# Kernel optimization log

Hardware: AMD Instinct MI355X
Metric: run time of the kernel (lower is better)

## Reference

```python
import jax, jax.numpy as jnp
import numpy as np

D_STATE = 64
D_CONV = 4
DT_RANK = 16  # ceil(256/16)
LN_EPS = 1e-5


def _mamba_layer(x, ln_g, ln_b, in_w, conv_w, conv_b, xp_w, dt_w, dt_b, A_log, Dp, out_w):
    B, L, d_model = x.shape
    # LayerNorm (pre-norm)
    mu = x.mean(-1, keepdims=True)
    var = ((x - mu) ** 2).mean(-1, keepdims=True)
    xn = (x - mu) * jax.lax.rsqrt(var + LN_EPS) * ln_g + ln_b
    # in_proj -> split into x-branch and gate z
    xz = xn @ in_w.T                    # [B,L,2*d_inner]
    xm, z = jnp.split(xz, 2, axis=-1)   # each [B,L,d_inner]
    d_inner = xm.shape[-1]
    # causal depthwise conv1d (kernel D_CONV), then SiLU
    xp = jnp.pad(xm, ((0, 0), (D_CONV - 1, 0), (0, 0)))
    xc = conv_b + sum(xp[:, k:k + L, :] * conv_w[:, k] for k in range(D_CONV))
    xc = jax.nn.silu(xc)
    # input-dependent SSM params
    dbl = xc @ xp_w.T                   # [B,L,dt_rank+2*N]
    dt, Bm, Cm = jnp.split(dbl, [DT_RANK, DT_RANK + D_STATE], axis=-1)
    dt = jax.nn.softplus(dt @ dt_w.T + dt_b)   # [B,L,d_inner]
    A = -jnp.exp(A_log)                 # [d_inner, N]

    def step(h, inp):
        dt_t, B_t, C_t, u_t = inp       # [B,Di],[B,N],[B,N],[B,Di]
        dA = jnp.exp(dt_t[:, :, None] * A)                 # [B,Di,N]
        dBu = (dt_t * u_t)[:, :, None] * B_t[:, None, :]   # [B,Di,N]
        h = dA * h + dBu
        y = jnp.einsum('bdn,bn->bd', h, C_t)
        return h, y

    h0 = jnp.zeros((B, d_inner, D_STATE), x.dtype)
    _, ys = jax.lax.scan(
        step, h0,
        (dt.transpose(1, 0, 2), Bm.transpose(1, 0, 2), Cm.transpose(1, 0, 2), xc.transpose(1, 0, 2)))
    y = ys.transpose(1, 0, 2) + xc * Dp  # skip term D*u
    y = y * jax.nn.silu(z)               # gating
    out = y @ out_w.T                    # out_proj
    return out + x                       # residual


def reference(x, ln_g, ln_b, in_w, conv_w, conv_b, xp_w, dt_w, dt_b, A_log, Dp, out_w):
    depth = ln_g.shape[0]
    for i in range(depth):
        x = _mamba_layer(x, ln_g[i], ln_b[i], in_w[i], conv_w[i], conv_b[i],
                         xp_w[i], dt_w[i], dt_b[i], A_log[i], Dp[i], out_w[i])
    return x


def setup_inputs() -> dict:
    key = jax.random.key(0)
    ks = jax.random.split(key, 8)
    B, L, d_model, depth = 4, 1024, 256, 2
    d_inner = 2 * d_model
    x = jax.random.normal(ks[0], (B, L, d_model), jnp.float32)
    s = 0.02
    in_w = jax.random.normal(ks[1], (depth, 2 * d_inner, d_model), jnp.float32) * s
    conv_w = jax.random.normal(ks[2], (depth, d_inner, D_CONV), jnp.float32) * 0.3
    conv_b = jnp.zeros((depth, d_inner), jnp.float32)
    xp_w = jax.random.normal(ks[3], (depth, DT_RANK + 2 * D_STATE, d_inner), jnp.float32) * s
    dt_w = jax.random.normal(ks[4], (depth, d_inner, DT_RANK), jnp.float32) * 0.1
    # inverse-softplus of ~0.01 so dt starts small (mamba-style init)
    dt_b = jnp.full((depth, d_inner), float(np.log(np.expm1(0.01))), jnp.float32)
    # A = diag(1..N) per channel -> A_log = log(arange)
    A_log = jnp.broadcast_to(jnp.log(jnp.arange(1, D_STATE + 1, dtype=jnp.float32)),
                             (depth, d_inner, D_STATE))
    Dp = jnp.ones((depth, d_inner), jnp.float32)
    out_w = jax.random.normal(ks[5], (depth, d_model, d_inner), jnp.float32) * s
    ln_g = jnp.ones((depth, d_model), jnp.float32)
    ln_b = jnp.zeros((depth, d_model), jnp.float32)
    return {"x": x, "ln_g": ln_g, "ln_b": ln_b, "in_w": in_w, "conv_w": conv_w,
            "conv_b": conv_b, "xp_w": xp_w, "dt_w": dt_w, "dt_b": dt_b,
            "A_log": A_log, "Dp": Dp, "out_w": out_w}
```

## Files before the change

### kernel.cpp

```cpp
#include <hip/hip_runtime.h>
#include <math.h>

#define DI 512
#define DM 256
#define LSEQ 1024
#define BB 4
#define NST 64
#define ROWS (BB*LSEQ)
#define NC 16
#define CL 64

typedef __bf16 bf16x8 __attribute__((ext_vector_type(8)));
typedef __bf16 bf16x4 __attribute__((ext_vector_type(4)));
typedef float f32x4 __attribute__((ext_vector_type(4)));
typedef unsigned short u16;
typedef u16 u16x8 __attribute__((ext_vector_type(8)));

__device__ __forceinline__ float siluf(float x) { return x / (1.f + __expf(-x)); }
__device__ __forceinline__ float softplusf(float x) { return (x > 20.f) ? x : log1pf(__expf(x)); }
__device__ __forceinline__ float rlane(float v, int l) {
    return __int_as_float(__builtin_amdgcn_readlane(__float_as_int(v), l));
}
__device__ __forceinline__ float fexp2(float x) {
#if __has_builtin(__builtin_amdgcn_exp2f)
    return __builtin_amdgcn_exp2f(x);
#else
    return __expf(x * 0.69314718056f);
#endif
}

__device__ __forceinline__ float tree8(const float (&s)[8], int lane) {
    const bool b5 = (lane & 32) != 0;
    const bool b4 = (lane & 16) != 0;
    const bool b3 = (lane & 8) != 0;
    float r[4];
    #pragma unroll
    for (int i = 0; i < 4; ++i) {
        float u = b5 ? s[i+4] : s[i];
        float w = b5 ? s[i]   : s[i+4];
        r[i] = u + __shfl_xor(w, 32, 64);
    }
    float q[2];
    #pragma unroll
    for (int i = 0; i < 2; ++i) {
        float u = b4 ? r[i+2] : r[i];
        float w = b4 ? r[i]   : r[i+2];
        q[i] = u + __shfl_xor(w, 16, 64);
    }
    float u = b3 ? q[1] : q[0];
    float w = b3 ? q[0] : q[1];
    float p = u + __shfl_xor(w, 8, 64);
    p += __shfl_xor(p, 4, 64);
    p += __shfl_xor(p, 2, 64);
    p += __shfl_xor(p, 1, 64);
    return p;
}

__global__ __launch_bounds__(256) void f2bf(
    const float* __restrict__ in, __bf16* __restrict__ out, int n)
{
    int i = (blockIdx.x * 256 + threadIdx.x) * 4;
    if (i >= n) return;
    float4 v = *(const float4*)(in + i);
    bf16x4 o;
    o[0] = (__bf16)v.x; o[1] = (__bf16)v.y; o[2] = (__bf16)v.z; o[3] = (__bf16)v.w;
    *(bf16x4*)(out + i) = o;
}

__global__ __launch_bounds__(256) void ln_kernel(
    const float* __restrict__ x, const float* __restrict__ g,
    const float* __restrict__ b, __bf16* __restrict__ xn)
{
    int lane = threadIdx.x & 63;
    int row = blockIdx.x * 4 + (threadIdx.x >> 6);
    const float4* xr = (const float4*)(x + (size_t)row * DM);
    float4 v = xr[lane];
    float s = v.x + v.y + v.z + v.w;
    #pragma unroll
    for (int o = 32; o; o >>= 1) s += __shfl_xor(s, o, 64);
    float mu = s * (1.f / DM);
    float dx = v.x - mu, dy = v.y - mu, dz = v.z - mu, dw = v.w - mu;
    float q = dx*dx + dy*dy + dz*dz + dw*dw;
    #pragma unroll
    for (int o = 32; o; o >>= 1) q += __shfl_xor(q, o, 64);
    float inv = rsqrtf(q * (1.f / DM) + 1e-5f);
    float4 gv = ((const float4*)g)[lane];
    float4 bv = ((const float4*)b)[lane];
    bf16x4 o4;
    o4[0] = (__bf16)(dx * inv * gv.x + bv.x);
    o4[1] = (__bf16)(dy * inv * gv.y + bv.y);
    o4[2] = (__bf16)(dz * inv * gv.z + bv.z);
    o4[3] = (__bf16)(dw * inv * gv.w + bv.w);
    *(bf16x4*)(xn + (size_t)row * DM + lane * 4) = o4;
}

template<int KK>
__global__ __launch_bounds__(256) void gemm_mfma(
    const __bf16* __restrict__ A, const __bf16* __restrict__ W,
    float* __restrict__ C, __bf16* __restrict__ C2b,
    const float* __restrict__ res, int N, int mode)
{
    int wid = threadIdx.x >> 6, lane = threadIdx.x & 63;
    int wr = wid >> 1, wc = wid & 1;
    int bm = blockIdx.y * 128, bn = blockIdx.x * 64;
    int l15 = lane & 15, lk = (lane >> 4) * 8;
    const __bf16* Ap = A + (size_t)(bm + wr*64 + l15) * KK + lk;
    int wrow0 = bn + wc*32 + l15;
    int wrow1 = wrow0 + 16;
    if (wrow0 > N-1) wrow0 = N-1;
    if (wrow1 > N-1) wrow1 = N-1;
    const __bf16* Wp0 = W + (size_t)wrow0 * KK + lk;
    const __bf16* Wp1 = W + (size_t)wrow1 * KK + lk;
    f32x4 acc[4][2] = {};
    #pragma unroll 4
    for (int k0 = 0; k0 < KK; k0 += 32) {
        bf16x8 b0 = *(const bf16x8*)(Wp0 + k0);
        bf16x8 b1 = *(const bf16x8*)(Wp1 + k0);
        #pragma unroll
        for (int m = 0; m < 4; ++m) {
            bf16x8 a = *(const bf16x8*)(Ap + (size_t)m*16*KK + k0);
            acc[m][0] = __builtin_amdgcn_mfma_f32_16x16x32_bf16(a, b0, acc[m][0], 0, 0, 0);
            acc[m][1] = __builtin_amdgcn_mfma_f32_16x16x32_bf16(a, b1, acc[m][1], 0, 0, 0);
        }
    }
    int r4 = (lane >> 4) * 4;
    #pragma unroll
    for (int m = 0; m < 4; ++m) {
        int row = bm + wr*64 + m*16 + r4;
        #pragma unroll
        for (int n = 0; n < 2; ++n) {
            int col = bn + wc*32 + n*16 + l15;
            #pragma unroll
            for (int r = 0; r < 4; ++r) {
                float v = acc[m][n][r];
                int rr = row + r;
                if (mode == 0) {
                    if (col < N) C[(size_t)rr * N + col] = v;
                } else if (mode == 1) {
                    if (col < 512) C[(size_t)rr * 512 + col] = v;
                    else           C2b[(size_t)rr * 512 + col - 512] = (__bf16)v;
                } else {
                    C[(size_t)rr * N + col] = v + res[(size_t)rr * N + col];
                }
            }
        }
    }
}

__global__ __launch_bounds__(256) void gemm_dt(
    const float* __restrict__ A, int lda,
    const float* __restrict__ W,
    float* __restrict__ CT, const float* __restrict__ aux)
{
    __shared__ float As[16][68];
    __shared__ float Ws[16][68];
    const int bm = blockIdx.y * 64;
    const int bn = blockIdx.x * 64;
    const int tid = threadIdx.x;
    const int tx = tid & 15;
    const int ty = tid >> 4;
    const int lr = tid >> 2;
    const int lc = (tid & 3) << 2;
    float acc[4][4] = {};

    {
        float4 av = *(const float4*)(A + (size_t)(bm + lr) * lda + lc);
        float4 wv = *(const float4*)(W + (size_t)(bn + lr) * 16 + lc);
        As[lc+0][lr] = av.x; As[lc+1][lr] = av.y; As[lc+2][lr] = av.z; As[lc+3][lr] = av.w;
        Ws[lc+0][lr] = wv.x; Ws[lc+1][lr] = wv.y; Ws[lc+2][lr] = wv.z; Ws[lc+3][lr] = wv.w;
        __syncthreads();
        #pragma unroll
        for (int k = 0; k < 16; ++k) {
            float a[4], w[4];
            #pragma unroll
            for (int i = 0; i < 4; ++i) a[i] = As[k][ty*4 + i];
            #pragma unroll
            for (int j = 0; j < 4; ++j) w[j] = Ws[k][tx*4 + j];
            #pragma unroll
            for (int i = 0; i < 4; ++i)
                #pragma unroll
                for (int j = 0; j < 4; ++j)
                    acc[i][j] = fmaf(a[i], w[j], acc[i][j]);
        }
    }

    #pragma unroll
    for (int j = 0; j < 4; ++j) {
        int n = bn + tx*4 + j;
        float bia = aux[n];
        float4 v;
        v.x = softplusf(acc[0][j] + bia);
        v.y = softplusf(acc[1][j] + bia);
        v.z = softplusf(acc[2][j] + bia);
        v.w = softplusf(acc[3][j] + bia);
        *(float4*)(CT + (size_t)n * ROWS + bm + ty*4) = v;
    }
}

__global__ __launch_bounds__(256) void conv_silu_kernel(
    const float* __restrict__ xm, const float* __restrict__ cw,
    const float* __restrict__ cb, __bf16* __restrict__ xcb)
{
    int idx = blockIdx.x * 256 + threadIdx.x;
    int d = idx & (DI - 1);
    int row = idx >> 9;
    int t = row & (LSEQ - 1);
    float w0 = cw[d*4+0], w1 = cw[d*4+1], w2 = cw[d*4+2], w3 = cw[d*4+3];
    float acc = cb[d];
    const float* p = xm + (size_t)row * DI + d;
    if (t >= 3) {
        acc += p[-3*DI]*w0 + p[-2*DI]*w1 + p[-1*DI]*w2 + p[0]*w3;
    } else {
        if (t >= 2) acc += p[-2*DI]*w1;
        if (t >= 1) acc += p[-1*DI]*w2;
        acc += p[0]*w3;
    }
    xcb[idx] = (__bf16)siluf(acc);
}

__global__ __launch_bounds__(256) void transpose_bf(
    const u16* __restrict__ in, u16* __restrict__ out, int ldi, int ldo)
{
    __shared__ u16 tile[64][72];
    int r = threadIdx.x >> 2;
    int c0 = (threadIdx.x & 3) * 16;
    const u16* ip = in + (size_t)(blockIdx.y*64 + r) * ldi + blockIdx.x*64 + c0;
    *(u16x8*)&tile[r][c0]     = *(const u16x8*)(ip);
    *(u16x8*)&tile[r][c0 + 8] = *(const u16x8*)(ip + 8);
    __syncthreads();
    u16* op = out + (size_t)(blockIdx.x*64 + r) * ldo + blockIdx.y*64 + c0;
    u16x8 v0, v1;
    #pragma unroll
    for (int i = 0; i < 8; ++i) { v0[i] = tile[c0+i][r]; v1[i] = tile[c0+8+i][r]; }
    *(u16x8*)(op)     = v0;
    *(u16x8*)(op + 8) = v1;
}

__global__ __launch_bounds__(256) void scan_p1T(
    const float* __restrict__ dtT, const __bf16* __restrict__ xcT,
    const float* __restrict__ dbl, const float* __restrict__ A_log,
    float* __restrict__ Pe, float* __restrict__ He)
{
    int wid = (blockIdx.x * 256 + threadIdx.x) >> 6;
    int lane = threadIdx.x & 63;
    int c = wid & (NC - 1);
    int d = (wid >> 4) & (DI - 1);
    int b = wid >> 13;
    float An2 = -__expf(A_log[d * NST + lane]) * 1.44269504f;
    size_t row0 = (size_t)b * LSEQ + (size_t)c * CL;
    size_t tix = (size_t)d * ROWS + row0;
    float dtv = dtT[tix + lane];
    float uvf = (float)xcT[tix + lane];
    float duv = dtv * uvf;
    const float* bp = dbl + row0 * 144 + 16 + lane;
    float P = 1.f, H = 0.f;
    float Bv[8], Bn[8];
    #pragma unroll
    for (int q = 0; q < 8; ++q) Bv[q] = bp[q * 144];
    #pragma unroll
    for (int j = 0; j < 8; ++j) {
        if (j < 7) {
            #pragma unroll
            for (int q = 0; q < 8; ++q) Bn[q] = bp[(8*j + 8 + q) * 144];
        }
        #pragma unroll
        for (int q = 0; q < 8; ++q) {
            const int t = 8*j + q;
            float dA = fexp2(rlane(dtv, t) * An2);
            P *= dA;
            H = fmaf(dA, H, rlane(duv, t) * Bv[q]);
        }
        #pragma unroll
        for (int q = 0; q < 8; ++q) Bv[q] = Bn[q];
    }
    size_t o = (size_t)wid * 64 + lane;
    Pe[o] = P;
    He[o] = H;
}

__global__ __launch_bounds__(256) void scan_carry(
    float* __restrict__ Pe, const float* __restrict__ He)
{
    int wid = (blockIdx.x * 256 + threadIdx.x) >> 6;
    int lane = threadIdx.x & 63;
    size_t base = (size_t)wid * NC * 64 + lane;
    float p[15], q[15];
    #pragma unroll
    for (int j = 0; j < 15; ++j) {
        p[j] = Pe[base + (size_t)j * 64];
        q[j] = He[base + (size_t)j * 64];
    }
    float h = 0.f;
    #pragma unroll
    for (int j = 0; j < 15; ++j) {
        h = fmaf(p[j], h, q[j]);
        Pe[base + (size_t)j * 64] = h;
    }
}

__global__ __launch_bounds__(256) void scan_p2T(
    const float* __restrict__ dtT, const __bf16* __restrict__ xcT,
    const __bf16* __restrict__ zT, const float* __restrict__ dbl,
    const float* __restrict__ A_log, const float* __restrict__ Dp,
    const float* __restrict__ Pe, __bf16* __restrict__ yT)
{
    __shared__ float Ys[4][64];
    int wid = (blockIdx.x * 256 + threadIdx.x) >> 6;
    int w = threadIdx.x >> 6;
    int lane = threadIdx.x & 63;
    int c = wid & (NC - 1);
    int d = (wid >> 4) & (DI - 1);
    int b = wid >> 13;
    float An2 = -__expf(A_log[d * NST + lane]) * 1.44269504f;
    size_t row0 = (size_t)b * LSEQ + (size_t)c * CL;
    size_t tix = (size_t)d * ROWS + row0;
    float dtv = dtT[tix + lane];
    float uvf = (float)xcT[tix + lane];
    float zvf = (float)zT[tix + lane];
    float duv = dtv * uvf;
    float gD  = uvf * Dp[d];
    float wz  = siluf(zvf);
    float h = (c == 0) ? 0.f : Pe[(size_t)(wid - 1) * 64 + lane];
    const float* bp = dbl + row0 * 144 + 16 + lane;
    const float* cp = dbl + row0 * 144 + 80 + lane;
    float Bv[8], Cv[8], Bn[8], Cn[8];
    #pragma unroll
    for (int q = 0; q < 8; ++q) { Bv[q] = bp[q*144]; Cv[q] = cp[q*144]; }
    float yred[8];
    #pragma unroll
    for (int j = 0; j < 8; ++j) {
        if (j < 7) {
            #pragma unroll
            for (int q = 0; q < 8; ++q) {
                Bn[q] = bp[(8*j + 8 + q) * 144];
                Cn[q] = cp[(8*j + 8 + q) * 144];
            }
        }
        float s[8];
        #pragma unroll
        for (int q = 0; q < 8; ++q) {
            const int t = 8*j + q;
            float dA = fexp2(rlane(dtv, t) * An2);
            h = fmaf(dA, h, rlane(duv, t) * Bv[q]);
            s[q] = h * Cv[q];
        }
        yred[j] = tree8(s, lane);
        #pragma unroll
        for (int q = 0; q < 8; ++q) { Bv[q] = Bn[q]; Cv[q] = Cn[q]; }
    }
    if ((lane & 7) == 0) {
        #pragma unroll
        for (int j = 0; j < 8; ++j) Ys[w][8*j + (lane >> 3)] = yred[j];
    }
    float y = (Ys[w][lane] + gD) * wz;
    yT[tix + lane] = (__bf16)y;
}

extern "C" void kernel_launch(void* const* d_in, const int* in_sizes, int n_in,
                              void* d_out, int out_size, void* d_ws, size_t ws_size,
                              hipStream_t stream)
{
    const float* x      = (const float*)d_in[0];
    const float* ln_g   = (const float*)d_in[1];
    const float* ln_b   = (const float*)d_in[2];
    const float* in_w   = (const float*)d_in[3];
    const float* conv_w = (const float*)d_in[4];
    const float* conv_b = (const float*)d_in[5];
    const float* xp_w   = (const float*)d_in[6];
    const float* dt_w   = (const float*)d_in[7];
    const float* dt_b   = (const float*)d_in[8];
    const float* A_log  = (const float*)d_in[9];
    const float* Dp     = (const float*)d_in[10];
    const float* out_w  = (const float*)d_in[11];
    float* out = (float*)d_out;

    char* ws = (char*)d_ws;
    const size_t MB = 1u << 20;
    float*  xm   = (float*)(ws + 0*MB);
    float*  Pe   = (float*)(ws + 0*MB);
    float*  dtT  = (float*)(ws + 8*MB);
    __bf16* xcbf = (__bf16*)(ws + 16*MB);
    __bf16* yTb  = (__bf16*)(ws + 16*MB);
    __bf16* xcT  = (__bf16*)(ws + 20*MB);
    __bf16* zbf  = (__bf16*)(ws + 24*MB);
    __bf16* ybf  = (__bf16*)(ws + 24*MB);
    __bf16* zT   = (__bf16*)(ws + 28*MB);
    float*  He   = (float*)(ws + 32*MB);
    float*  dblb = (float*)(ws + 40*MB);
    __bf16* xnb  = (__bf16*)(ws + 43*MB);
    __bf16* w_in  = (__bf16*)(ws + 45*MB);
    __bf16* w_xp  = (__bf16*)(ws + 46*MB);
    __bf16* w_out = (__bf16*)(ws + 46*MB + 512*1024);

    f2bf<<<512, 256, 0, stream>>>(in_w,  w_in,  2*1024*DM);
    f2bf<<<144, 256, 0, stream>>>(xp_w,  w_xp,  2*144*DI);
    f2bf<<<256, 256, 0, stream>>>(out_w, w_out, 2*DM*DI);

    for (int l = 0; l < 2; ++l) {
        const float* xin = (l == 0) ? x : out;
        ln_kernel<<<ROWS/4, 256, 0, stream>>>(xin, ln_g + l*DM, ln_b + l*DM, xnb);
        gemm_mfma<DM><<<dim3(1024/64, ROWS/128), 256, 0, stream>>>(
            xnb, w_in + (size_t)l*1024*DM, xm, zbf, nullptr, 1024, 1);
        conv_silu_kernel<<<(ROWS*DI)/256, 256, 0, stream>>>(
            xm, conv_w + (size_t)l*DI*4, conv_b + (size_t)l*DI, xcbf);
        gemm_mfma<DI><<<dim3(3, ROWS/128), 256, 0, stream>>>(
            xcbf, w_xp + (size_t)l*144*DI, dblb, nullptr, nullptr, 144, 0);
        transpose_bf<<<dim3(DI/64, ROWS/64), 256, 0, stream>>>(
            (const u16*)xcbf, (u16*)xcT, DI, ROWS);
        transpose_bf<<<dim3(DI/64, ROWS/64), 256, 0, stream>>>(
            (const u16*)zbf, (u16*)zT, DI, ROWS);
        gemm_dt<<<dim3(DI/64, ROWS/64), 256, 0, stream>>>(
            dblb, 144, dt_w + (size_t)l*DI*16, dtT, dt_b + (size_t)l*DI);
        scan_p1T<<<(BB*DI*NC)/4, 256, 0, stream>>>(
            dtT, xcT, dblb, A_log + (size_t)l*DI*NST, Pe, He);
        scan_carry<<<(BB*DI)/4, 256, 0, stream>>>(Pe, He);
        scan_p2T<<<(BB*DI*NC)/4, 256, 0, stream>>>(
            dtT, xcT, zT, dblb, A_log + (size_t)l*DI*NST, Dp + (size_t)l*DI,
            Pe, yTb);
        transpose_bf<<<dim3(ROWS/64, DI/64), 256, 0, stream>>>(
            (const u16*)yTb, (u16*)ybf, ROWS, DI);
        gemm_mfma<DI><<<dim3(DM/64, ROWS/128), 256, 0, stream>>>(
            ybf, w_out + (size_t)l*DM*DI, out, nullptr, xin, DM, 2);
    }
}
```

Before: 356.3 us.

## Shrink GEMM M-tile, compute chunk decay via dt sum, drop manual B/C prefetch

The MFMA GEMM row tile is halved from 128 to 64, doubling the grid to raise occupancy and CU coverage at the cost of less A/W reuse per block. In the first scan pass the running product of per-step decays is replaced by a single exp2 of A times the chunk's summed dt, computed with a wave shuffle reduction, which removes a multiply per step. Both scan kernels drop their hand-written double-buffered register prefetch of B and C and load directly inside the loop, leaving load scheduling to the compiler. The closed-form decay differs slightly in rounding from the multiplied product.

```diff
diff --git a/kernel.cpp b/kernel.cpp
--- a/kernel.cpp
+++ b/kernel.cpp
@@ -102,22 +102,22 @@
 {
     int wid = threadIdx.x >> 6, lane = threadIdx.x & 63;
     int wr = wid >> 1, wc = wid & 1;
-    int bm = blockIdx.y * 128, bn = blockIdx.x * 64;
+    int bm = blockIdx.y * 64, bn = blockIdx.x * 64;
     int l15 = lane & 15, lk = (lane >> 4) * 8;
-    const __bf16* Ap = A + (size_t)(bm + wr*64 + l15) * KK + lk;
+    const __bf16* Ap = A + (size_t)(bm + wr*32 + l15) * KK + lk;
     int wrow0 = bn + wc*32 + l15;
     int wrow1 = wrow0 + 16;
     if (wrow0 > N-1) wrow0 = N-1;
     if (wrow1 > N-1) wrow1 = N-1;
     const __bf16* Wp0 = W + (size_t)wrow0 * KK + lk;
     const __bf16* Wp1 = W + (size_t)wrow1 * KK + lk;
-    f32x4 acc[4][2] = {};
+    f32x4 acc[2][2] = {};
     #pragma unroll 4
     for (int k0 = 0; k0 < KK; k0 += 32) {
         bf16x8 b0 = *(const bf16x8*)(Wp0 + k0);
         bf16x8 b1 = *(const bf16x8*)(Wp1 + k0);
         #pragma unroll
-        for (int m = 0; m < 4; ++m) {
+        for (int m = 0; m < 2; ++m) {
             bf16x8 a = *(const bf16x8*)(Ap + (size_t)m*16*KK + k0);
             acc[m][0] = __builtin_amdgcn_mfma_f32_16x16x32_bf16(a, b0, acc[m][0], 0, 0, 0);
             acc[m][1] = __builtin_amdgcn_mfma_f32_16x16x32_bf16(a, b1, acc[m][1], 0, 0, 0);
@@ -125,8 +125,8 @@
     }
     int r4 = (lane >> 4) * 4;
     #pragma unroll
-    for (int m = 0; m < 4; ++m) {
-        int row = bm + wr*64 + m*16 + r4;
+    for (int m = 0; m < 2; ++m) {
+        int row = bm + wr*32 + m*16 + r4;
         #pragma unroll
         for (int n = 0; n < 2; ++n) {
             int col = bn + wc*32 + n*16 + l15;
@@ -252,29 +252,23 @@
     float dtv = dtT[tix + lane];
     float uvf = (float)xcT[tix + lane];
     float duv = dtv * uvf;
+    float Sdt = dtv;
+    #pragma unroll
+    for (int o = 32; o; o >>= 1) Sdt += __shfl_xor(Sdt, o, 64);
     const float* bp = dbl + row0 * 144 + 16 + lane;
-    float P = 1.f, H = 0.f;
-    float Bv[8], Bn[8];
-    #pragma unroll
-    for (int q = 0; q < 8; ++q) Bv[q] = bp[q * 144];
+    float H = 0.f;
     #pragma unroll
     for (int j = 0; j < 8; ++j) {
-        if (j < 7) {
-            #pragma unroll
-            for (int q = 0; q < 8; ++q) Bn[q] = bp[(8*j + 8 + q) * 144];
-        }
         #pragma unroll
         for (int q = 0; q < 8; ++q) {
             const int t = 8*j + q;
             float dA = fexp2(rlane(dtv, t) * An2);
-            P *= dA;
-            H = fmaf(dA, H, rlane(duv, t) * Bv[q]);
+            H = fmaf(dA, H, rlane(duv, t) * bp[q * 144]);
         }
-        #pragma unroll
-        for (int q = 0; q < 8; ++q) Bv[q] = Bn[q];
+        bp += 8 * 144;
     }
     size_t o = (size_t)wid * 64 + lane;
-    Pe[o] = P;
+    Pe[o] = fexp2(An2 * Sdt);
     He[o] = H;
 }
 
@@ -323,30 +317,20 @@
     float h = (c == 0) ? 0.f : Pe[(size_t)(wid - 1) * 64 + lane];
     const float* bp = dbl + row0 * 144 + 16 + lane;
     const float* cp = dbl + row0 * 144 + 80 + lane;
-    float Bv[8], Cv[8], Bn[8], Cn[8];
-    #pragma unroll
-    for (int q = 0; q < 8; ++q) { Bv[q] = bp[q*144]; Cv[q] = cp[q*144]; }
     float yred[8];
     #pragma unroll
     for (int j = 0; j < 8; ++j) {
-        if (j < 7) {
-            #pragma unroll
-            for (int q = 0; q < 8; ++q) {
-                Bn[q] = bp[(8*j + 8 + q) * 144];
-                Cn[q] = cp[(8*j + 8 + q) * 144];
-            }
-        }
         float s[8];
         #pragma unroll
         for (int q = 0; q < 8; ++q) {
             const int t = 8*j + q;
             float dA = fexp2(rlane(dtv, t) * An2);
-            h = fmaf(dA, h, rlane(duv, t) * Bv[q]);
-            s[q] = h * Cv[q];
+            h = fmaf(dA, h, rlane(duv, t) * bp[q * 144]);
+            s[q] = h * cp[q * 144];
         }
         yred[j] = tree8(s, lane);
-        #pragma unroll
-        for (int q = 0; q < 8; ++q) { Bv[q] = Bn[q]; Cv[q] = Cn[q]; }
+        bp += 8 * 144;
+        cp += 8 * 144;
     }
     if ((lane & 7) == 0) {
         #pragma unroll
@@ -399,11 +383,11 @@
     for (int l = 0; l < 2; ++l) {
         const float* xin = (l == 0) ? x : out;
         ln_kernel<<<ROWS/4, 256, 0, stream>>>(xin, ln_g + l*DM, ln_b + l*DM, xnb);
-        gemm_mfma<DM><<<dim3(1024/64, ROWS/128), 256, 0, stream>>>(
+        gemm_mfma<DM><<<dim3(1024/64, ROWS/64), 256, 0, stream>>>(
             xnb, w_in + (size_t)l*1024*DM, xm, zbf, nullptr, 1024, 1);
         conv_silu_kernel<<<(ROWS*DI)/256, 256, 0, stream>>>(
             xm, conv_w + (size_t)l*DI*4, conv_b + (size_t)l*DI, xcbf);
-        gemm_mfma<DI><<<dim3(3, ROWS/128), 256, 0, stream>>>(
+        gemm_mfma<DI><<<dim3(3, ROWS/64), 256, 0, stream>>>(
             xcbf, w_xp + (size_t)l*144*DI, dblb, nullptr, nullptr, 144, 0);
         transpose_bf<<<dim3(DI/64, ROWS/64), 256, 0, stream>>>(
             (const u16*)xcbf, (u16*)xcT, DI, ROWS);
@@ -419,7 +403,7 @@
             Pe, yTb);
         transpose_bf<<<dim3(ROWS/64, DI/64), 256, 0, stream>>>(
             (const u16*)yTb, (u16*)ybf, ROWS, DI);
-        gemm_mfma<DI><<<dim3(DM/64, ROWS/128), 256, 0, stream>>>(
+        gemm_mfma<DI><<<dim3(DM/64, ROWS/64), 256, 0, stream>>>(
             ybf, w_out + (size_t)l*DM*DI, out, nullptr, xin, DM, 2);
     }
 }
```

Result: faster. 325.5 us (-8.6%).
